# Kernel tuning notes

Measured on AMD Instinct MI355X. Metric: run time of the kernel, lower is better.

The kernel has to match this reference:

```python
import jax, jax.numpy as jnp
import numpy as np

D_MODEL = 1024
H = 16
D_K = 64
D_V = 64
NEG_INF = -1e9
LN_EPS = 1e-5


def setup_inputs() -> dict:
    key = jax.random.key(0)
    ks = jax.random.split(key, 7)
    B, S = 4, 2048
    scale = 1.0 / np.sqrt(D_MODEL)
    return {
        "Q": jax.random.normal(ks[0], (B, S, D_MODEL), jnp.float32),
        "K": jax.random.normal(ks[1], (B, S, D_MODEL), jnp.float32),
        "V": jax.random.normal(ks[2], (B, S, D_MODEL), jnp.float32),
        "W_Q": jax.random.normal(ks[3], (D_MODEL, D_K * H), jnp.float32) * scale,
        "W_K": jax.random.normal(ks[4], (D_MODEL, D_K * H), jnp.float32) * scale,
        "W_V": jax.random.normal(ks[5], (D_MODEL, D_V * H), jnp.float32) * scale,
        "W_O": jax.random.normal(ks[6], (D_V * H, D_MODEL), jnp.float32) * scale,
        "ln_gamma": jnp.ones((D_MODEL,), jnp.float32),
        "ln_beta": jnp.zeros((D_MODEL,), jnp.float32),
    }


def reference(Q, K, V, W_Q, W_K, W_V, W_O, ln_gamma, ln_beta):
    B, Lq, _ = Q.shape
    Lk = K.shape[1]
    # projections, split into heads: [B, H, L, d]
    Qh = (Q @ W_Q).reshape(B, Lq, H, D_K).transpose(0, 2, 1, 3)
    Kh = (K @ W_K).reshape(B, Lk, H, D_K).transpose(0, 2, 1, 3)
    Vh = (V @ W_V).reshape(B, Lk, H, D_V).transpose(0, 2, 1, 3)
    # scaled dot-product scores [B, H, Lq, Lk]
    scores = jnp.einsum("bhqd,bhkd->bhqk", Qh, Kh) / jnp.sqrt(jnp.float32(D_K))
    # causal mask: upper triangle (excl. diagonal) gets -1e9 added
    mask = jnp.triu(jnp.full((Lq, Lk), NEG_INF, jnp.float32), k=1)
    scores = scores + mask
    attn = jax.nn.softmax(scores, axis=-1)
    ctx = jnp.einsum("bhqk,bhkd->bhqd", attn, Vh)
    ctx = ctx.transpose(0, 2, 1, 3).reshape(B, Lq, H * D_V)
    out = ctx @ W_O
    # residual + layernorm
    x = Q + out
    mu = jnp.mean(x, axis=-1, keepdims=True)
    var = jnp.mean(jnp.square(x - mu), axis=-1, keepdims=True)
    return (x - mu) * jax.lax.rsqrt(var + LN_EPS) * ln_gamma + ln_beta
```

## Files before the change

kernel.cpp:

```cpp
#include <hip/hip_runtime.h>
#include <cstdint>
#include <cstddef>

#define DM  1024
#define SEQ 2048
#define BATCH 4
#define NH  16
#define DH  64
#define QKS 2048

typedef __bf16 bf16_t;
typedef __bf16 bf16x8 __attribute__((ext_vector_type(8)));
typedef __bf16 bf16x4 __attribute__((ext_vector_type(4)));
typedef float  f32x4  __attribute__((ext_vector_type(4)));

#define MFMA16(a, b, c) __builtin_amdgcn_mfma_f32_16x16x32_bf16((a), (b), (c), 0, 0, 0)

#define CS 0.18033688f

#define ASYNC_COPY16(gsrc, ldst)                                                   \
  __builtin_amdgcn_global_load_lds(                                                \
      (__attribute__((address_space(1))) void*)(gsrc),                             \
      (__attribute__((address_space(3))) void*)(ldst), 16, 0, 0)

#define NCVT (3 * BATCH * SEQ * DM / 4 / 256)

__global__ __launch_bounds__(256) void prep_kernel(const float* __restrict__ Q,
                                                   const float* __restrict__ K,
                                                   const float* __restrict__ V,
                                                   const float* __restrict__ W0,
                                                   const float* __restrict__ W1,
                                                   const float* __restrict__ W2,
                                                   const float* __restrict__ W3,
                                                   bf16_t* __restrict__ Qb,
                                                   bf16_t* __restrict__ Kb,
                                                   bf16_t* __restrict__ Vb,
                                                   bf16_t* __restrict__ WTall) {
  __shared__ float tile[32][33];
  const int bid = blockIdx.x;
  if (bid < NCVT) {
    const int n4 = BATCH * SEQ * DM / 4;
    int i = bid * 256 + threadIdx.x;
    const float* src; bf16_t* dst; int j;
    if (i < n4)           { src = Q; dst = Qb; j = i; }
    else if (i < 2 * n4)  { src = K; dst = Kb; j = i - n4; }
    else                  { src = V; dst = Vb; j = i - 2 * n4; }
    float4 v = ((const float4*)src)[j];
    bf16x4 o;
    o[0] = (bf16_t)v.x; o[1] = (bf16_t)v.y; o[2] = (bf16_t)v.z; o[3] = (bf16_t)v.w;
    *(bf16x4*)(dst + (size_t)j * 4) = o;
    return;
  }
  const int wb = bid - NCVT;
  const int widx = wb >> 10, wid = wb & 1023;
  const float* W = (widx == 0) ? W0 : (widx == 1) ? W1 : (widx == 2) ? W2 : W3;
  bf16_t* WT = WTall + (size_t)widx * DM * DM;
  const int bn = wid & 31, bk = wid >> 5;
  const int tx = threadIdx.x & 31, ty = threadIdx.x >> 5;
#pragma unroll
  for (int r = 0; r < 4; ++r)
    tile[ty + r * 8][tx] = W[(size_t)(bk * 32 + ty + r * 8) * DM + bn * 32 + tx];
  __syncthreads();
#pragma unroll
  for (int r = 0; r < 4; ++r)
    WT[(size_t)(bn * 32 + ty + r * 8) * DM + bk * 32 + tx] = (bf16_t)tile[tx][ty + r * 8];
}

__global__ __launch_bounds__(256) void gemm_bt_kernel(const bf16_t* __restrict__ A0,
                                                      const bf16_t* __restrict__ A1,
                                                      const bf16_t* __restrict__ A2,
                                                      const bf16_t* __restrict__ BT,
                                                      bf16_t* __restrict__ C,
                                                      bf16_t* __restrict__ Vtr,
                                                      int K, int ldc,
                                                      float qscale, int qcols) {
  __shared__ bf16_t Sh[4][128 * 32];
  const int tid = threadIdx.x;
  const int wv = tid >> 6, lane = tid & 63;
  const int lo = lane & 15, quad = lane >> 4;

  const int bid = blockIdx.x;
  const int xcd = bid & 7;
  const int rid = bid >> 3;
  const int m0 = (xcd * 8 + (rid & 7)) * 128;
  const int n0 = (rid >> 3) * 128;
  const int wm = wv & 1, wn = wv >> 1;

  const bf16_t* A = (n0 < 1024) ? A0 : (n0 < 2048) ? A1 : A2;
  const float sc = (n0 < qcols) ? qscale : 1.0f;

  f32x4 acc[4][4] = {};

  const int srow = wv * 32 + (lane >> 2);
  const int scol = (lane & 3) * 8;
  const bf16_t* Ag = A + (size_t)(m0 + srow) * K + scol;
  const bf16_t* Bg = BT + (size_t)(n0 + srow) * K + scol;
  const int lds_off = (wv * 32) * 32;

  ASYNC_COPY16(Ag, Sh[0] + lds_off);
  ASYNC_COPY16(Ag + (size_t)16 * K, Sh[0] + lds_off + 16 * 32);
  ASYNC_COPY16(Bg, Sh[2] + lds_off);
  ASYNC_COPY16(Bg + (size_t)16 * K, Sh[2] + lds_off + 16 * 32);

  const int kiters = K >> 5;
  for (int ki = 0; ki < kiters; ++ki) {
    const int cur = ki & 1;
    __syncthreads();
    if (ki + 1 < kiters) {
      const int k1 = (ki + 1) << 5;
      ASYNC_COPY16(Ag + k1, Sh[cur ^ 1] + lds_off);
      ASYNC_COPY16(Ag + k1 + (size_t)16 * K, Sh[cur ^ 1] + lds_off + 16 * 32);
      ASYNC_COPY16(Bg + k1, Sh[2 + (cur ^ 1)] + lds_off);
      ASYNC_COPY16(Bg + k1 + (size_t)16 * K, Sh[2 + (cur ^ 1)] + lds_off + 16 * 32);
    }

    bf16x8 af[4], bfr[4];
#pragma unroll
    for (int t = 0; t < 4; ++t) {
      af[t]  = *(const bf16x8*)(Sh[cur] + (wm * 64 + t * 16 + lo) * 32 + quad * 8);
      bfr[t] = *(const bf16x8*)(Sh[2 + cur] + (wn * 64 + t * 16 + lo) * 32 + quad * 8);
    }
#pragma unroll
    for (int mt = 0; mt < 4; ++mt)
#pragma unroll
      for (int nt = 0; nt < 4; ++nt)
        acc[mt][nt] = MFMA16(af[mt], bfr[nt], acc[mt][nt]);
  }

  __syncthreads();

  if (Vtr != nullptr && n0 >= 2048) {
    bf16_t* Tw = &Sh[wv][0];
#pragma unroll
    for (int nt = 0; nt < 4; ++nt) {
      const int row = nt * 16 + lo;
#pragma unroll
      for (int mt = 0; mt < 4; ++mt) {
        const int cb = mt * 16 + quad * 4;
        bf16x4 pk;
#pragma unroll
        for (int r = 0; r < 4; ++r) pk[r] = (bf16_t)acc[mt][nt][r];
        *(bf16x4*)(Tw + row * 64 + (((cb >> 3) ^ (row & 7)) * 8) + (cb & 7)) = pk;
      }
    }
    __asm__ volatile("s_waitcnt lgkmcnt(0)" ::: "memory");
    const int h  = ((n0 - 2048) >> 6) + wn;
    const int mg = m0 + wm * 64;
    const int b  = mg >> 11;
    const int s0 = mg & (SEQ - 1);
    const int dr = lane >> 3, ck = lane & 7;
    bf16_t* vbase = Vtr + ((size_t)((b * NH + h) * DH)) * SEQ + s0;
#pragma unroll
    for (int pass = 0; pass < 8; ++pass) {
      const int d = pass * 8 + dr;
      const bf16x8 vv = *(const bf16x8*)(Tw + d * 64 + ((ck ^ (d & 7)) * 8));
      *(bf16x8*)(vbase + (size_t)d * SEQ + ck * 8) = vv;
    }
    return;
  }

#pragma unroll
  for (int mt = 0; mt < 4; ++mt)
#pragma unroll
    for (int nt = 0; nt < 4; ++nt)
#pragma unroll
      for (int r = 0; r < 4; ++r) {
        const int m = m0 + wm * 64 + mt * 16 + quad * 4 + r;
        const int n = n0 + wn * 64 + nt * 16 + lo;
        C[(size_t)m * ldc + n] = (bf16_t)(acc[mt][nt][r] * sc);
      }
}

__global__ __launch_bounds__(256) void attn_kernel(const bf16_t* __restrict__ QKV,
                                                   const bf16_t* __restrict__ Vt,
                                                   bf16_t* __restrict__ ctx) {
  __shared__ bf16_t Ks[2][64 * 64];
  __shared__ bf16_t Vs[2][64 * 64];
  __shared__ bf16_t Ps[4][2][16 * 64];
  const int tid = threadIdx.x;
  const int wv = tid >> 6, lane = tid & 63;
  const int lo = lane & 15, quad = lane >> 4;
  const int bh = blockIdx.x & 63;
  const int pid = blockIdx.x >> 6;
  const int b = bh >> 4, h = bh & 15;

  const bf16_t* Qg = QKV + ((size_t)b * SEQ) * QKS + h * DH;
  const bf16_t* Kg = QKV + ((size_t)b * SEQ) * QKS + 1024 + h * DH;
  const bf16_t* Vg = Vt + ((size_t)(bh * DH)) * SEQ;

  const int U0 = wv * 128 + lane, U1 = U0 + 64;
  const int r0 = U0 >> 3, cg0 = (U0 & 7) ^ (r0 & 7);
  const int r1 = U1 >> 3, cg1 = (U1 & 7) ^ (r1 & 7);

  bf16_t* PwA = &Ps[wv][0][0];
  bf16_t* PwB = &Ps[wv][1][0];
  const int pwr_base = lo * 64;
  const int prd0 = lo * 64 + ((quad ^ (lo & 7)) * 8);
  const int prd1 = lo * 64 + (((4 + quad) ^ (lo & 7)) * 8);

  for (int half = 0; half < 2; ++half) {
    const int qblk = half ? (15 - pid) : pid;
    const int jmax = 2 * qblk + 1;
    const int qw = qblk * 128 + wv * 16;
    const int qgA = qw + lo;
    const int qgB = qgA + 64;

    const bf16_t* Qba = Qg + ((size_t)qgA) * QKS + quad * 8;
    const bf16x8 aQ0A = *(const bf16x8*)(Qba);
    const bf16x8 aQ1A = *(const bf16x8*)(Qba + 32);
    const bf16_t* Qbb = Qba + (size_t)64 * QKS;
    const bf16x8 aQ0B = *(const bf16x8*)(Qbb);
    const bf16x8 aQ1B = *(const bf16x8*)(Qbb + 32);

    f32x4 OA[4] = {}, OB[4] = {};
    float lA = 0.0f, lB = 0.0f;

    __syncthreads();
    ASYNC_COPY16(Kg + (size_t)r0 * QKS + cg0 * 8, Ks[0] + (wv * 2 + 0) * 512);
    ASYNC_COPY16(Kg + (size_t)r1 * QKS + cg1 * 8, Ks[0] + (wv * 2 + 1) * 512);
    ASYNC_COPY16(Vg + (size_t)r0 * SEQ + cg0 * 8, Vs[0] + (wv * 2 + 0) * 512);
    ASYNC_COPY16(Vg + (size_t)r1 * SEQ + cg1 * 8, Vs[0] + (wv * 2 + 1) * 512);

    for (int jtp = 0; jtp <= jmax; jtp += 2) {
#pragma unroll
      for (int u = 0; u < 2; ++u) {
        const int jt = jtp + u;
        __syncthreads();
        if (jt < jmax) {
          const int j1 = (jt + 1) * 64;
          ASYNC_COPY16(Kg + (size_t)(j1 + r0) * QKS + cg0 * 8, Ks[u ^ 1] + (wv * 2 + 0) * 512);
          ASYNC_COPY16(Kg + (size_t)(j1 + r1) * QKS + cg1 * 8, Ks[u ^ 1] + (wv * 2 + 1) * 512);
          ASYNC_COPY16(Vg + (size_t)r0 * SEQ + j1 + cg0 * 8, Vs[u ^ 1] + (wv * 2 + 0) * 512);
          ASYNC_COPY16(Vg + (size_t)r1 * SEQ + j1 + cg1 * 8, Vs[u ^ 1] + (wv * 2 + 1) * 512);
        }

        const int j0 = jt * 64;
        const bool aact = (jt != jmax);
        const bool diagA = (jt == jmax - 1);
        const bool diagB = (jt == jmax);

        f32x4 sA[4], sB[4];
#pragma unroll
        for (int mt = 0; mt < 4; ++mt) {
          const int row = mt * 16 + lo;
          const bf16x8 k0 = *(const bf16x8*)(Ks[u] + row * 64 + ((quad ^ (row & 7)) * 8));
          const bf16x8 k1 = *(const bf16x8*)(Ks[u] + row * 64 + (((4 + quad) ^ (row & 7)) * 8));
          if (aact) {
            f32x4 s = {};
            s = MFMA16(k0, aQ0A, s);
            s = MFMA16(k1, aQ1A, s);
            sA[mt] = s;
          }
          f32x4 t = {};
          t = MFMA16(k0, aQ0B, t);
          t = MFMA16(k1, aQ1B, t);
          sB[mt] = t;
        }

        if (aact) {
          float ls = 0.0f;
#pragma unroll
          for (int mt = 0; mt < 4; ++mt) {
            bf16x4 pk;
#pragma unroll
            for (int r = 0; r < 4; ++r) {
              float s = sA[mt][r];
              if (diagA && (j0 + mt * 16 + quad * 4 + r > qgA)) s = -1e30f;
              const float p = __builtin_amdgcn_exp2f(s);
              ls += p;
              pk[r] = (bf16_t)p;
            }
            const int sp = (mt * 2 + (quad >> 1)) ^ (lo & 7);
            *(bf16x4*)(PwA + pwr_base + sp * 8 + (quad & 1) * 4) = pk;
          }
          ls += __shfl_xor(ls, 16);
          ls += __shfl_xor(ls, 32);
          lA += ls;
        }
        {
          float ls = 0.0f;
#pragma unroll
          for (int mt = 0; mt < 4; ++mt) {
            bf16x4 pk;
#pragma unroll
            for (int r = 0; r < 4; ++r) {
              float s = sB[mt][r];
              if (diagB && (j0 + mt * 16 + quad * 4 + r > qgB)) s = -1e30f;
              const float p = __builtin_amdgcn_exp2f(s);
              ls += p;
              pk[r] = (bf16_t)p;
            }
            const int sp = (mt * 2 + (quad >> 1)) ^ (lo & 7);
            *(bf16x4*)(PwB + pwr_base + sp * 8 + (quad & 1) * 4) = pk;
          }
          ls += __shfl_xor(ls, 16);
          ls += __shfl_xor(ls, 32);
          lB += ls;
        }

        __asm__ volatile("s_waitcnt lgkmcnt(0)" ::: "memory");
        bf16x8 pA0, pA1;
        if (aact) {
          pA0 = *(const bf16x8*)(PwA + prd0);
          pA1 = *(const bf16x8*)(PwA + prd1);
        }
        const bf16x8 pB0 = *(const bf16x8*)(PwB + prd0);
        const bf16x8 pB1 = *(const bf16x8*)(PwB + prd1);

#pragma unroll
        for (int nt = 0; nt < 4; ++nt) {
          const int row = nt * 16 + lo;
          const bf16x8 v0 = *(const bf16x8*)(Vs[u] + row * 64 + ((quad ^ (row & 7)) * 8));
          const bf16x8 v1 = *(const bf16x8*)(Vs[u] + row * 64 + (((4 + quad) ^ (row & 7)) * 8));
          if (aact) {
            OA[nt] = MFMA16(pA0, v0, OA[nt]);
            OA[nt] = MFMA16(pA1, v1, OA[nt]);
          }
          OB[nt] = MFMA16(pB0, v0, OB[nt]);
          OB[nt] = MFMA16(pB1, v1, OB[nt]);
        }
      }
    }

    float invA[4], invB[4];
#pragma unroll
    for (int r = 0; r < 4; ++r) {
      invA[r] = 1.0f / __shfl(lA, quad * 4 + r);
      invB[r] = 1.0f / __shfl(lB, quad * 4 + r);
    }
    bf16_t* outp = ctx + ((size_t)(b * SEQ + qw + quad * 4)) * DM + h * DH + lo;
#pragma unroll
    for (int r = 0; r < 4; ++r)
#pragma unroll
      for (int nt = 0; nt < 4; ++nt) {
        outp[(size_t)r * DM + nt * 16] = (bf16_t)(OA[nt][r] * invA[r]);
        outp[(size_t)(r + 64) * DM + nt * 16] = (bf16_t)(OB[nt][r] * invB[r]);
      }
  }
}

__global__ __launch_bounds__(256) void ln_kernel(const float* __restrict__ Qin,
                                                 const bf16_t* __restrict__ Y,
                                                 const float* __restrict__ gamma,
                                                 const float* __restrict__ beta,
                                                 float* __restrict__ out) {
  const int row = blockIdx.x, t = threadIdx.x;
  const float4 a = ((const float4*)(Qin + (size_t)row * DM))[t];
  const bf16x4 yv = ((const bf16x4*)(Y + (size_t)row * DM))[t];
  const float x0 = a.x + (float)yv[0], x1 = a.y + (float)yv[1];
  const float x2 = a.z + (float)yv[2], x3 = a.w + (float)yv[3];
  float s  = x0 + x1 + x2 + x3;
  float ss = x0 * x0 + x1 * x1 + x2 * x2 + x3 * x3;
#pragma unroll
  for (int off = 1; off < 64; off <<= 1) { s += __shfl_xor(s, off); ss += __shfl_xor(ss, off); }
  __shared__ float red[8];
  const int wv = t >> 6, lane = t & 63;
  if (lane == 0) { red[wv * 2] = s; red[wv * 2 + 1] = ss; }
  __syncthreads();
  s  = red[0] + red[2] + red[4] + red[6];
  ss = red[1] + red[3] + red[5] + red[7];
  const float mu  = s * (1.0f / DM);
  const float var = ss * (1.0f / DM) - mu * mu;
  const float rstd = rsqrtf(var + 1e-5f);
  const float4 g  = ((const float4*)gamma)[t];
  const float4 be = ((const float4*)beta)[t];
  float4 o;
  o.x = (x0 - mu) * rstd * g.x + be.x;
  o.y = (x1 - mu) * rstd * g.y + be.y;
  o.z = (x2 - mu) * rstd * g.z + be.z;
  o.w = (x3 - mu) * rstd * g.w + be.w;
  ((float4*)(out + (size_t)row * DM))[t] = o;
}

extern "C" void kernel_launch(void* const* d_in, const int* in_sizes, int n_in,
                              void* d_out, int out_size, void* d_ws, size_t ws_size,
                              hipStream_t stream) {
  const float* Q     = (const float*)d_in[0];
  const float* K     = (const float*)d_in[1];
  const float* V     = (const float*)d_in[2];
  const float* W_Q   = (const float*)d_in[3];
  const float* W_K   = (const float*)d_in[4];
  const float* W_V   = (const float*)d_in[5];
  const float* W_O   = (const float*)d_in[6];
  const float* gamma = (const float*)d_in[7];
  const float* beta  = (const float*)d_in[8];
  float* out = (float*)d_out;

  char* ws = (char*)d_ws;
  const size_t SZB = (size_t)BATCH * SEQ * DM * 2;
  const size_t WTB = (size_t)DM * DM * 2;
  bf16_t* Qb    = (bf16_t*)(ws);
  bf16_t* Kb    = (bf16_t*)(ws + SZB);
  bf16_t* Vb    = (bf16_t*)(ws + 2 * SZB);
  bf16_t* Yb    = (bf16_t*)(ws);
  bf16_t* WTall = (bf16_t*)(ws + 3 * SZB);
  char* p2 = ws + 3 * SZB + 4 * WTB;
  bf16_t* QKV = (bf16_t*)(p2);
  bf16_t* Vtr = (bf16_t*)(p2 + 2 * SZB);
  bf16_t* ctx = (bf16_t*)(p2 + 3 * SZB);

  prep_kernel<<<NCVT + 4096, 256, 0, stream>>>(Q, K, V, W_Q, W_K, W_V, W_O,
                                               Qb, Kb, Vb, WTall);

  gemm_bt_kernel<<<(3072 / 128) * (BATCH * SEQ / 128), 256, 0, stream>>>(
      Qb, Kb, Vb, WTall, QKV, Vtr, DM, QKS, CS, 1024);

  attn_kernel<<<64 * 8, 256, 0, stream>>>(QKV, Vtr, ctx);

  gemm_bt_kernel<<<(DM / 128) * (BATCH * SEQ / 128), 256, 0, stream>>>(
      ctx, ctx, ctx, WTall + (size_t)3 * DM * DM, Yb, nullptr, DM, DM, 1.0f, 0);
  ln_kernel<<<BATCH * SEQ, 256, 0, stream>>>(Q, Yb, gamma, beta, out);
}
```

Measured before the change: 314.3 us.

## Split causal q-block pairs into separate blocks and share P scratch buffer

The attention kernel now launches one block per 128-row query block (1024 blocks) instead of pairing a light and a heavy q-block per block (512 blocks). The mapping interleaves heavy and light blocks so the dispatcher sees a balanced mix. The two per-wave P scratch buffers are merged into one, with the B-half probabilities held in registers until the A-half is read back, halving that LDS use. It also adds a 4-blocks-per-CU launch bound to raise occupancy, at the risk of register pressure and less balance inside each block.

New measurement: 317.7 us. No clear change (+1.1%).

```diff
diff --git a/kernel.cpp b/kernel.cpp
--- a/kernel.cpp
+++ b/kernel.cpp
@@ -171,17 +171,18 @@
       }
 }
 
-__global__ __launch_bounds__(256) void attn_kernel(const bf16_t* __restrict__ QKV,
-                                                   const bf16_t* __restrict__ Vt,
-                                                   bf16_t* __restrict__ ctx) {
+__global__ __launch_bounds__(256, 4) void attn_kernel(const bf16_t* __restrict__ QKV,
+                                                      const bf16_t* __restrict__ Vt,
+                                                      bf16_t* __restrict__ ctx) {
   __shared__ bf16_t Ks[2][64 * 64];
   __shared__ bf16_t Vs[2][64 * 64];
-  __shared__ bf16_t Ps[4][2][16 * 64];
+  __shared__ bf16_t Ps[4][16 * 64];
   const int tid = threadIdx.x;
   const int wv = tid >> 6, lane = tid & 63;
   const int lo = lane & 15, quad = lane >> 4;
   const int bh = blockIdx.x & 63;
-  const int pid = blockIdx.x >> 6;
+  const int u16 = blockIdx.x >> 6;
+  const int qblk = (u16 & 1) ? ((u16 - 1) >> 1) : (15 - (u16 >> 1));
   const int b = bh >> 4, h = bh & 15;
 
   const bf16_t* Qg = QKV + ((size_t)b * SEQ) * QKS + h * DH;
@@ -192,151 +193,150 @@
   const int r0 = U0 >> 3, cg0 = (U0 & 7) ^ (r0 & 7);
   const int r1 = U1 >> 3, cg1 = (U1 & 7) ^ (r1 & 7);
 
-  bf16_t* PwA = &Ps[wv][0][0];
-  bf16_t* PwB = &Ps[wv][1][0];
+  bf16_t* Pw = &Ps[wv][0];
   const int pwr_base = lo * 64;
   const int prd0 = lo * 64 + ((quad ^ (lo & 7)) * 8);
   const int prd1 = lo * 64 + (((4 + quad) ^ (lo & 7)) * 8);
 
-  for (int half = 0; half < 2; ++half) {
-    const int qblk = half ? (15 - pid) : pid;
-    const int jmax = 2 * qblk + 1;
-    const int qw = qblk * 128 + wv * 16;
-    const int qgA = qw + lo;
-    const int qgB = qgA + 64;
-
-    const bf16_t* Qba = Qg + ((size_t)qgA) * QKS + quad * 8;
-    const bf16x8 aQ0A = *(const bf16x8*)(Qba);
-    const bf16x8 aQ1A = *(const bf16x8*)(Qba + 32);
-    const bf16_t* Qbb = Qba + (size_t)64 * QKS;
-    const bf16x8 aQ0B = *(const bf16x8*)(Qbb);
-    const bf16x8 aQ1B = *(const bf16x8*)(Qbb + 32);
-
-    f32x4 OA[4] = {}, OB[4] = {};
-    float lA = 0.0f, lB = 0.0f;
-
-    __syncthreads();
-    ASYNC_COPY16(Kg + (size_t)r0 * QKS + cg0 * 8, Ks[0] + (wv * 2 + 0) * 512);
-    ASYNC_COPY16(Kg + (size_t)r1 * QKS + cg1 * 8, Ks[0] + (wv * 2 + 1) * 512);
-    ASYNC_COPY16(Vg + (size_t)r0 * SEQ + cg0 * 8, Vs[0] + (wv * 2 + 0) * 512);
-    ASYNC_COPY16(Vg + (size_t)r1 * SEQ + cg1 * 8, Vs[0] + (wv * 2 + 1) * 512);
-
-    for (int jtp = 0; jtp <= jmax; jtp += 2) {
-#pragma unroll
-      for (int u = 0; u < 2; ++u) {
-        const int jt = jtp + u;
-        __syncthreads();
-        if (jt < jmax) {
-          const int j1 = (jt + 1) * 64;
-          ASYNC_COPY16(Kg + (size_t)(j1 + r0) * QKS + cg0 * 8, Ks[u ^ 1] + (wv * 2 + 0) * 512);
-          ASYNC_COPY16(Kg + (size_t)(j1 + r1) * QKS + cg1 * 8, Ks[u ^ 1] + (wv * 2 + 1) * 512);
-          ASYNC_COPY16(Vg + (size_t)r0 * SEQ + j1 + cg0 * 8, Vs[u ^ 1] + (wv * 2 + 0) * 512);
-          ASYNC_COPY16(Vg + (size_t)r1 * SEQ + j1 + cg1 * 8, Vs[u ^ 1] + (wv * 2 + 1) * 512);
+  const int jmax = 2 * qblk + 1;
+  const int qw = qblk * 128 + wv * 16;
+  const int qgA = qw + lo;
+  const int qgB = qgA + 64;
+
+  const bf16_t* Qba = Qg + ((size_t)qgA) * QKS + quad * 8;
+  const bf16x8 aQ0A = *(const bf16x8*)(Qba);
+  const bf16x8 aQ1A = *(const bf16x8*)(Qba + 32);
+  const bf16_t* Qbb = Qba + (size_t)64 * QKS;
+  const bf16x8 aQ0B = *(const bf16x8*)(Qbb);
+  const bf16x8 aQ1B = *(const bf16x8*)(Qbb + 32);
+
+  f32x4 OA[4] = {}, OB[4] = {};
+  float lA = 0.0f, lB = 0.0f;
+
+  ASYNC_COPY16(Kg + (size_t)r0 * QKS + cg0 * 8, Ks[0] + (wv * 2 + 0) * 512);
+  ASYNC_COPY16(Kg + (size_t)r1 * QKS + cg1 * 8, Ks[0] + (wv * 2 + 1) * 512);
+  ASYNC_COPY16(Vg + (size_t)r0 * SEQ + cg0 * 8, Vs[0] + (wv * 2 + 0) * 512);
+  ASYNC_COPY16(Vg + (size_t)r1 * SEQ + cg1 * 8, Vs[0] + (wv * 2 + 1) * 512);
+
+  for (int jtp = 0; jtp <= jmax; jtp += 2) {
+#pragma unroll
+    for (int un = 0; un < 2; ++un) {
+      const int jt = jtp + un;
+      __syncthreads();
+      if (jt < jmax) {
+        const int j1 = (jt + 1) * 64;
+        ASYNC_COPY16(Kg + (size_t)(j1 + r0) * QKS + cg0 * 8, Ks[un ^ 1] + (wv * 2 + 0) * 512);
+        ASYNC_COPY16(Kg + (size_t)(j1 + r1) * QKS + cg1 * 8, Ks[un ^ 1] + (wv * 2 + 1) * 512);
+        ASYNC_COPY16(Vg + (size_t)r0 * SEQ + j1 + cg0 * 8, Vs[un ^ 1] + (wv * 2 + 0) * 512);
+        ASYNC_COPY16(Vg + (size_t)r1 * SEQ + j1 + cg1 * 8, Vs[un ^ 1] + (wv * 2 + 1) * 512);
+      }
+
+      const int j0 = jt * 64;
+      const bool aact = (jt != jmax);
+      const bool diagA = (jt == jmax - 1);
+      const bool diagB = (jt == jmax);
+
+      f32x4 sA[4], sB[4];
+#pragma unroll
+      for (int mt = 0; mt < 4; ++mt) {
+        const int row = mt * 16 + lo;
+        const bf16x8 k0 = *(const bf16x8*)(Ks[un] + row * 64 + ((quad ^ (row & 7)) * 8));
+        const bf16x8 k1 = *(const bf16x8*)(Ks[un] + row * 64 + (((4 + quad) ^ (row & 7)) * 8));
+        if (aact) {
+          f32x4 s = {};
+          s = MFMA16(k0, aQ0A, s);
+          s = MFMA16(k1, aQ1A, s);
+          sA[mt] = s;
         }
-
-        const int j0 = jt * 64;
-        const bool aact = (jt != jmax);
-        const bool diagA = (jt == jmax - 1);
-        const bool diagB = (jt == jmax);
-
-        f32x4 sA[4], sB[4];
+        f32x4 t = {};
+        t = MFMA16(k0, aQ0B, t);
+        t = MFMA16(k1, aQ1B, t);
+        sB[mt] = t;
+      }
+
+      if (aact) {
+        float ls = 0.0f;
 #pragma unroll
         for (int mt = 0; mt < 4; ++mt) {
-          const int row = mt * 16 + lo;
-          const bf16x8 k0 = *(const bf16x8*)(Ks[u] + row * 64 + ((quad ^ (row & 7)) * 8));
-          const bf16x8 k1 = *(const bf16x8*)(Ks[u] + row * 64 + (((4 + quad) ^ (row & 7)) * 8));
-          if (aact) {
-            f32x4 s = {};
-            s = MFMA16(k0, aQ0A, s);
-            s = MFMA16(k1, aQ1A, s);
-            sA[mt] = s;
+          bf16x4 pk;
+#pragma unroll
+          for (int r = 0; r < 4; ++r) {
+            float s = sA[mt][r];
+            if (diagA && (j0 + mt * 16 + quad * 4 + r > qgA)) s = -1e30f;
+            const float p = __builtin_amdgcn_exp2f(s);
+            ls += p;
+            pk[r] = (bf16_t)p;
           }
-          f32x4 t = {};
-          t = MFMA16(k0, aQ0B, t);
-          t = MFMA16(k1, aQ1B, t);
-          sB[mt] = t;
+          const int sp = (mt * 2 + (quad >> 1)) ^ (lo & 7);
+          *(bf16x4*)(Pw + pwr_base + sp * 8 + (quad & 1) * 4) = pk;
         }
-
+        ls += __shfl_xor(ls, 16);
+        ls += __shfl_xor(ls, 32);
+        lA += ls;
+      }
+
+      bf16x4 pkB[4];
+      {
+        float ls = 0.0f;
+#pragma unroll
+        for (int mt = 0; mt < 4; ++mt) {
+#pragma unroll
+          for (int r = 0; r < 4; ++r) {
+            float s = sB[mt][r];
+            if (diagB && (j0 + mt * 16 + quad * 4 + r > qgB)) s = -1e30f;
+            const float p = __builtin_amdgcn_exp2f(s);
+            ls += p;
+            pkB[mt][r] = (bf16_t)p;
+          }
+        }
+        ls += __shfl_xor(ls, 16);
+        ls += __shfl_xor(ls, 32);
+        lB += ls;
+      }
+
+      bf16x8 pA0, pA1;
+      if (aact) {
+        __asm__ volatile("s_waitcnt lgkmcnt(0)" ::: "memory");
+        pA0 = *(const bf16x8*)(Pw + prd0);
+        pA1 = *(const bf16x8*)(Pw + prd1);
+      }
+#pragma unroll
+      for (int mt = 0; mt < 4; ++mt) {
+        const int sp = (mt * 2 + (quad >> 1)) ^ (lo & 7);
+        *(bf16x4*)(Pw + pwr_base + sp * 8 + (quad & 1) * 4) = pkB[mt];
+      }
+      const bf16x8 pB0 = *(const bf16x8*)(Pw + prd0);
+      const bf16x8 pB1 = *(const bf16x8*)(Pw + prd1);
+
+#pragma unroll
+      for (int nt = 0; nt < 4; ++nt) {
+        const int row = nt * 16 + lo;
+        const bf16x8 v0 = *(const bf16x8*)(Vs[un] + row * 64 + ((quad ^ (row & 7)) * 8));
+        const bf16x8 v1 = *(const bf16x8*)(Vs[un] + row * 64 + (((4 + quad) ^ (row & 7)) * 8));
         if (aact) {
-          float ls = 0.0f;
-#pragma unroll
-          for (int mt = 0; mt < 4; ++mt) {
-            bf16x4 pk;
-#pragma unroll
-            for (int r = 0; r < 4; ++r) {
-              float s = sA[mt][r];
-              if (diagA && (j0 + mt * 16 + quad * 4 + r > qgA)) s = -1e30f;
-              const float p = __builtin_amdgcn_exp2f(s);
-              ls += p;
-              pk[r] = (bf16_t)p;
-            }
-            const int sp = (mt * 2 + (quad >> 1)) ^ (lo & 7);
-            *(bf16x4*)(PwA + pwr_base + sp * 8 + (quad & 1) * 4) = pk;
-          }
-          ls += __shfl_xor(ls, 16);
-          ls += __shfl_xor(ls, 32);
-          lA += ls;
+          OA[nt] = MFMA16(pA0, v0, OA[nt]);
+          OA[nt] = MFMA16(pA1, v1, OA[nt]);
         }
-        {
-          float ls = 0.0f;
-#pragma unroll
-          for (int mt = 0; mt < 4; ++mt) {
-            bf16x4 pk;
-#pragma unroll
-            for (int r = 0; r < 4; ++r) {
-              float s = sB[mt][r];
-              if (diagB && (j0 + mt * 16 + quad * 4 + r > qgB)) s = -1e30f;
-              const float p = __builtin_amdgcn_exp2f(s);
-              ls += p;
-              pk[r] = (bf16_t)p;
-            }
-            const int sp = (mt * 2 + (quad >> 1)) ^ (lo & 7);
-            *(bf16x4*)(PwB + pwr_base + sp * 8 + (quad & 1) * 4) = pk;
-          }
-          ls += __shfl_xor(ls, 16);
-          ls += __shfl_xor(ls, 32);
-          lB += ls;
-        }
-
-        __asm__ volatile("s_waitcnt lgkmcnt(0)" ::: "memory");
-        bf16x8 pA0, pA1;
-        if (aact) {
-          pA0 = *(const bf16x8*)(PwA + prd0);
-          pA1 = *(const bf16x8*)(PwA + prd1);
-        }
-        const bf16x8 pB0 = *(const bf16x8*)(PwB + prd0);
-        const bf16x8 pB1 = *(const bf16x8*)(PwB + prd1);
-
-#pragma unroll
-        for (int nt = 0; nt < 4; ++nt) {
-          const int row = nt * 16 + lo;
-          const bf16x8 v0 = *(const bf16x8*)(Vs[u] + row * 64 + ((quad ^ (row & 7)) * 8));
-          const bf16x8 v1 = *(const bf16x8*)(Vs[u] + row * 64 + (((4 + quad) ^ (row & 7)) * 8));
-          if (aact) {
-            OA[nt] = MFMA16(pA0, v0, OA[nt]);
-            OA[nt] = MFMA16(pA1, v1, OA[nt]);
-          }
-          OB[nt] = MFMA16(pB0, v0, OB[nt]);
-          OB[nt] = MFMA16(pB1, v1, OB[nt]);
-        }
-      }
-    }
-
-    float invA[4], invB[4];
-#pragma unroll
-    for (int r = 0; r < 4; ++r) {
-      invA[r] = 1.0f / __shfl(lA, quad * 4 + r);
-      invB[r] = 1.0f / __shfl(lB, quad * 4 + r);
-    }
-    bf16_t* outp = ctx + ((size_t)(b * SEQ + qw + quad * 4)) * DM + h * DH + lo;
-#pragma unroll
-    for (int r = 0; r < 4; ++r)
-#pragma unroll
-      for (int nt = 0; nt < 4; ++nt) {
-        outp[(size_t)r * DM + nt * 16] = (bf16_t)(OA[nt][r] * invA[r]);
-        outp[(size_t)(r + 64) * DM + nt * 16] = (bf16_t)(OB[nt][r] * invB[r]);
-      }
+        OB[nt] = MFMA16(pB0, v0, OB[nt]);
+        OB[nt] = MFMA16(pB1, v1, OB[nt]);
+      }
+    }
   }
+
+  float invA[4], invB[4];
+#pragma unroll
+  for (int r = 0; r < 4; ++r) {
+    invA[r] = 1.0f / __shfl(lA, quad * 4 + r);
+    invB[r] = 1.0f / __shfl(lB, quad * 4 + r);
+  }
+  bf16_t* outp = ctx + ((size_t)(b * SEQ + qw + quad * 4)) * DM + h * DH + lo;
+#pragma unroll
+  for (int r = 0; r < 4; ++r)
+#pragma unroll
+    for (int nt = 0; nt < 4; ++nt) {
+      outp[(size_t)r * DM + nt * 16] = (bf16_t)(OA[nt][r] * invA[r]);
+      outp[(size_t)(r + 64) * DM + nt * 16] = (bf16_t)(OB[nt][r] * invB[r]);
+    }
 }
 
 __global__ __launch_bounds__(256) void ln_kernel(const float* __restrict__ Qin,
@@ -405,7 +405,7 @@
   gemm_bt_kernel<<<(3072 / 128) * (BATCH * SEQ / 128), 256, 0, stream>>>(
       Qb, Kb, Vb, WTall, QKV, Vtr, DM, QKS, CS, 1024);
 
-  attn_kernel<<<64 * 8, 256, 0, stream>>>(QKV, Vtr, ctx);
+  attn_kernel<<<64 * 16, 256, 0, stream>>>(QKV, Vtr, ctx);
 
   gemm_bt_kernel<<<(DM / 128) * (BATCH * SEQ / 128), 256, 0, stream>>>(
       ctx, ctx, ctx, WTall + (size_t)3 * DM * DM, Yb, nullptr, DM, DM, 1.0f, 0);
```
